# Kernel tuning notes

Hardware: AMD Instinct MI355X
Metric: run time of the kernel (lower is better)

## Reference

```python
import jax, jax.numpy as jnp
import numpy as np

B, K, N, D = 2, 384, 4096, 1024      # batch, filtered spans, all spans, dim_span
H, L, DD, NB = 150, 12, 20, 10       # scorer hidden, n_labels, dist emb dim, n buckets
REL_PROP, RESIDUAL, CTXT_FF = 2, True, True


def setup_inputs() -> dict:
    key = jax.random.key(0)
    ks = jax.random.split(key, 14)
    span_vecs = jax.random.normal(ks[0], (B, K, D), dtype=jnp.float32)
    all_span_vecs = jax.random.normal(ks[1], (B, N, D), dtype=jnp.float32)
    span_begin = jnp.sort(jax.random.randint(ks[2], (B, K), 0, 512), axis=-1)
    span_end = span_begin + jax.random.randint(ks[3], (B, K), 0, 8)
    span_lengths = jnp.full((B,), (K * 9) // 10, dtype=jnp.int32)
    valid = jnp.arange(K)[None, :] < span_lengths[:, None]
    square_mask = (valid[:, :, None] & valid[:, None, :]).astype(jnp.float32)
    prune_indices = jnp.sort(jax.random.randint(ks[4], (B, K), 0, N), axis=-1)
    sequence_lengths = jnp.full((B,), 512, dtype=jnp.int32)
    p = lambda k, sh: jax.random.normal(k, sh, dtype=jnp.float32) * 0.02
    return {
        'span_vecs': span_vecs, 'all_span_vecs': all_span_vecs,
        'span_begin': span_begin, 'span_end': span_end,
        'square_mask': square_mask, 'prune_indices': prune_indices,
        'span_lengths': span_lengths, 'sequence_lengths': sequence_lengths,
        'Wl': p(ks[5], (D, H)), 'bl': jnp.zeros((H,), jnp.float32),
        'Wr': p(ks[6], (D, H)), 'br': jnp.zeros((H,), jnp.float32),
        'dist_emb': p(ks[7], (NB, DD)),
        'Wd': p(ks[8], (DD, H)), 'bd': jnp.zeros((H,), jnp.float32),
        'Wo': p(ks[9], (H, L)), 'bo': jnp.zeros((L,), jnp.float32),
        'Wff1': p(ks[10], (3 * D, D)), 'Wff2': p(ks[11], (D, D)),
        'Wg': p(ks[12], (2 * D, D)), 'bg': jnp.zeros((D,), jnp.float32),
    }


def _bucket(d):
    # coref-style distance buckets: 0..4 exact, then log2 buckets up to NB-1
    da = jnp.abs(d)
    lg = jnp.floor(jnp.log2(jnp.maximum(da, 1).astype(jnp.float32))).astype(jnp.int32) + 3
    return jnp.where(da <= 4, da, jnp.minimum(lg, NB - 1)).astype(jnp.int32)


def _scorer(u, span_begin, span_end, Wl, bl, Wr, br, dist_emb, Wd, bd, Wo, bo):
    # OptFFpairs: pairwise FF scorer, [B,K,D] -> [B,K,K,L] (dropout = identity, eval mode)
    l = u @ Wl + bl                                          # [B,K,H]
    r = u @ Wr + br                                          # [B,K,H]
    dist = span_begin[:, None, :] - span_end[:, :, None]     # [B,K,K]
    d = dist_emb[_bucket(dist)] @ Wd + bd                    # [B,K,K,H]
    h = jax.nn.relu(l[:, :, None, :] + r[:, None, :, :] + d)
    return h @ Wo + bo                                       # [B,K,K,L]


def _forward(span_vecs, square_mask, span_begin, span_end,
             Wl, bl, Wr, br, dist_emb, Wd, bd, Wo, bo, Wff1, Wff2, Wg, bg):
    u = span_vecs
    scores = _scorer(u, span_begin, span_end, Wl, bl, Wr, br, dist_emb, Wd, bd, Wo, bo)
    for _ in range(REL_PROP):
        probs1 = jax.nn.sigmoid(scores.max(-1)) * square_mask       # [B,K,K]
        probs2 = jnp.swapaxes(probs1, 1, 2)
        ctxt1 = jnp.einsum('bij,bjd->bid', probs1, u) / (probs1.sum(-1) + 1e-7)[..., None]
        ctxt2 = jnp.einsum('bij,bjd->bid', probs2, u) / (probs2.sum(-1) + 1e-7)[..., None]
        if CTXT_FF:
            ctxt = jnp.tanh(jnp.concatenate((u, ctxt1, ctxt2), -1) @ Wff1) @ Wff2
        else:
            ctxt = ctxt1 + ctxt2
        g = jax.nn.sigmoid(jnp.concatenate((u, ctxt), -1) @ Wg + bg)  # MyGate
        u = g * u + (1.0 - g) * ctxt
        new_scores = _scorer(u, span_begin, span_end, Wl, bl, Wr, br, dist_emb, Wd, bd, Wo, bo)
        scores = scores + new_scores if RESIDUAL else new_scores
    return u, scores


def reference(span_vecs, all_span_vecs, span_begin, span_end, square_mask,
              prune_indices, span_lengths, sequence_lengths,
              Wl, bl, Wr, br, dist_emb, Wd, bd, Wo, bo, Wff1, Wff2, Wg, bg):
    u, scores = _forward(span_vecs, square_mask, span_begin, span_end,
                         Wl, bl, Wr, br, dist_emb, Wd, bd, Wo, bo, Wff1, Wff2, Wg, bg)
    # overwrite_spans: write updated filtered span vecs back into all-span tensor
    valid = jnp.arange(K)[None, :] < span_lengths[:, None]          # [B,K]
    bidx = jnp.broadcast_to(jnp.arange(B)[:, None], (B, K))
    cur = all_span_vecs[bidx, prune_indices]                        # [B,K,D]
    vals = jnp.where(valid[..., None], u, cur)                      # invalid -> no-op write
    update_all = all_span_vecs.at[bidx, prune_indices].set(vals)
    return update_all, u, scores
```

## Files before the change

kernel.cpp:

```cpp
#include <hip/hip_runtime.h>
#include <math.h>

constexpr int Bc = 2, Kc = 384, Nc = 4096, Dc = 1024;
constexpr int Hc = 150, Lc = 12, DDc = 20, NBc = 10;
constexpr int Mrows = Bc * Kc;

typedef __attribute__((ext_vector_type(8))) unsigned short ushort8;
typedef __attribute__((ext_vector_type(8))) short short8;
typedef __attribute__((ext_vector_type(4))) float f32x4;

__device__ __forceinline__ float sigmoidf_(float x) { return 1.0f / (1.0f + expf(-x)); }

__device__ __forceinline__ unsigned short f2b(float f) {
    unsigned u = __float_as_uint(f);
    unsigned r = (u + 0x7fffu + ((u >> 16) & 1u)) >> 16;
    return (unsigned short)r;
}
__device__ __forceinline__ float b2f(unsigned short u) {
    return __uint_as_float((unsigned)u << 16);
}

__global__ __launch_bounds__(256) void cvt_k(const float* __restrict__ s,
                                             unsigned short* __restrict__ d, int n) {
    for (int i = blockIdx.x * 256 + threadIdx.x; i < n; i += gridDim.x * 256)
        d[i] = f2b(s[i]);
}

__global__ __launch_bounds__(256) void dtab_k(const float* __restrict__ de,
                                              const float* __restrict__ Wd,
                                              const float* __restrict__ bd,
                                              float* __restrict__ dtab) {
    int idx = blockIdx.x * 256 + threadIdx.x;
    if (idx >= NBc * Hc) return;
    int n = idx / Hc, h = idx - n * Hc;
    float s = bd[h];
#pragma unroll
    for (int k = 0; k < DDc; ++k) s = fmaf(de[n * DDc + k], Wd[k * Hc + h], s);
    dtab[n * Hc + h] = s;
}

__global__ __launch_bounds__(256) void trw_k(const float* __restrict__ Wsrc,
                                             unsigned short* __restrict__ WT,
                                             int K, int N) {
    __shared__ unsigned short t[32][33];
    const int k0 = blockIdx.y * 32, n0 = blockIdx.x * 32;
    const int tx = threadIdx.x & 31, ty = threadIdx.x >> 5;
#pragma unroll
    for (int i = 0; i < 4; ++i)
        t[ty + i * 8][tx] = f2b(Wsrc[(size_t)(k0 + ty + i * 8) * N + n0 + tx]);
    __syncthreads();
#pragma unroll
    for (int i = 0; i < 4; ++i)
        WT[(size_t)(n0 + ty + i * 8) * K + k0 + tx] = t[tx][ty + i * 8];
}

__global__ __launch_bounds__(256) void trwlr_k(const float* __restrict__ Wl,
                                               const float* __restrict__ Wr,
                                               const float* __restrict__ bl,
                                               const float* __restrict__ br,
                                               unsigned short* __restrict__ WlrT,
                                               float* __restrict__ blr) {
    int idx = blockIdx.x * 256 + threadIdx.x;
    if (idx < Hc) { blr[idx] = bl[idx]; blr[Hc + idx] = br[idx]; }
    if (idx >= 2 * Hc * Dc) return;
    int r = idx >> 10, k = idx & 1023;
    float v = (r < Hc) ? Wl[(size_t)k * Hc + r] : Wr[(size_t)k * Hc + (r - Hc)];
    WlrT[idx] = f2b(v);
}

__global__ __launch_bounds__(256) void trb_k(const unsigned short* __restrict__ src,
                                             unsigned short* __restrict__ dst,
                                             int R, int C, long sBatch, long dBatch) {
    __shared__ unsigned short t[32][33];
    const int z = blockIdx.z;
    src += (size_t)z * sBatch;
    dst += (size_t)z * dBatch;
    const int r0 = blockIdx.y * 32, c0 = blockIdx.x * 32;
    const int tx = threadIdx.x & 31, ty = threadIdx.x >> 5;
#pragma unroll
    for (int i = 0; i < 4; ++i)
        t[ty + i * 8][tx] = src[(size_t)(r0 + ty + i * 8) * C + c0 + tx];
    __syncthreads();
#pragma unroll
    for (int i = 0; i < 4; ++i)
        dst[(size_t)(c0 + ty + i * 8) * R + r0 + tx] = t[tx][ty + i * 8];
}

template <int NSRC, int EPI, bool SPLITK, bool BTRANS>
__global__ __launch_bounds__(256) void mfma3(
    const unsigned short* __restrict__ a0, const unsigned short* __restrict__ a1,
    const unsigned short* __restrict__ a2, int arstride, long aBatch,
    const unsigned short* __restrict__ Bm, int bstride, long wBatch, int wmask,
    int N, int Kd, int chunk,
    const float* __restrict__ rs, long rsBatch,
    float* __restrict__ outf, unsigned short* __restrict__ outb, long oBatch) {
    constexpr int LDA = 72;
    __shared__ unsigned short Als[2][64 * LDA];
    __shared__ unsigned short Bls[2][64 * LDA];

    const int z = blockIdx.z;
    int kbeg;
    if (SPLITK) {
        kbeg = z * chunk;
        outf += (size_t)z * oBatch;
    } else {
        kbeg = 0;
        chunk = Kd;
        a0 += (size_t)z * aBatch;
        Bm += (size_t)(z & wmask) * wBatch;
        if (rs) rs += (size_t)z * rsBatch;
        if (outb) outb += (size_t)z * oBatch;
    }
    const int kend = kbeg + chunk;

    const int tid = threadIdx.x;
    const int wave = tid >> 6, lane = tid & 63;
    const int wr = wave >> 1, wc = wave & 1;
    const int l15 = lane & 15, lg = lane >> 4;
    const int row0 = blockIdx.y * 64, col0 = blockIdx.x * 64;
    const int srow = tid >> 2, skc = (tid & 3) * 16;

    f32x4 acc[2][2] = {};
    ushort8 ra0, ra1, rb0, rb1;

#define LOAD_SLAB(kb)                                                                  \
    {                                                                                  \
        int kglob = (kb) + skc;                                                        \
        const unsigned short* asrc = a0;                                               \
        int kl = kglob;                                                                \
        if (NSRC > 1) {                                                                \
            int s = kglob >> 10;                                                       \
            kl = kglob & 1023;                                                         \
            asrc = (s == 0) ? a0 : ((s == 1 || NSRC == 2) ? a1 : a2);                  \
        }                                                                              \
        const unsigned short* p = asrc + (size_t)(row0 + srow) * arstride + kl;        \
        ra0 = *(const ushort8*)p;                                                      \
        ra1 = *(const ushort8*)(p + 8);                                                \
        if (BTRANS) {                                                                  \
            const unsigned short* q = Bm + (size_t)((kb) + srow) * bstride + col0 + skc; \
            rb0 = *(const ushort8*)q;                                                  \
            rb1 = *(const ushort8*)(q + 8);                                            \
        } else {                                                                       \
            int col = col0 + srow;                                                     \
            if (col < N) {                                                             \
                const unsigned short* q = Bm + (size_t)col * bstride + kglob;          \
                rb0 = *(const ushort8*)q;                                              \
                rb1 = *(const ushort8*)(q + 8);                                        \
            } else {                                                                   \
                ushort8 z8 = {};                                                       \
                rb0 = z8;                                                              \
                rb1 = z8;                                                              \
            }                                                                          \
        }                                                                              \
    }

#define WRITE_SLAB(b)                                                                  \
    {                                                                                  \
        *(ushort8*)&Als[b][srow * LDA + skc] = ra0;                                    \
        *(ushort8*)&Als[b][srow * LDA + skc + 8] = ra1;                                \
        if (BTRANS) {                                                                  \
            _Pragma("unroll") for (int j = 0; j < 8; ++j)                              \
                Bls[b][(skc + j) * LDA + srow] = rb0[j];                               \
            _Pragma("unroll") for (int j = 0; j < 8; ++j)                              \
                Bls[b][(skc + 8 + j) * LDA + srow] = rb1[j];                           \
        } else {                                                                       \
            *(ushort8*)&Bls[b][srow * LDA + skc] = rb0;                                \
            *(ushort8*)&Bls[b][srow * LDA + skc + 8] = rb1;                            \
        }                                                                              \
    }

    LOAD_SLAB(kbeg);
    WRITE_SLAB(0);
    __syncthreads();

    int cur = 0;
    for (int k0 = kbeg; k0 < kend; k0 += 64) {
        const bool more = (k0 + 64 < kend);
        if (more) LOAD_SLAB(k0 + 64);
#pragma unroll
        for (int h = 0; h < 2; ++h) {
            short8 af0 = *(const short8*)&Als[cur][(wr * 32 + l15) * LDA + h * 32 + lg * 8];
            short8 af1 = *(const short8*)&Als[cur][(wr * 32 + 16 + l15) * LDA + h * 32 + lg * 8];
            short8 bf0 = *(const short8*)&Bls[cur][(wc * 32 + l15) * LDA + h * 32 + lg * 8];
            short8 bf1 = *(const short8*)&Bls[cur][(wc * 32 + 16 + l15) * LDA + h * 32 + lg * 8];
            acc[0][0] = __builtin_amdgcn_mfma_f32_16x16x32_bf16(af0, bf0, acc[0][0], 0, 0, 0);
            acc[0][1] = __builtin_amdgcn_mfma_f32_16x16x32_bf16(af0, bf1, acc[0][1], 0, 0, 0);
            acc[1][0] = __builtin_amdgcn_mfma_f32_16x16x32_bf16(af1, bf0, acc[1][0], 0, 0, 0);
            acc[1][1] = __builtin_amdgcn_mfma_f32_16x16x32_bf16(af1, bf1, acc[1][1], 0, 0, 0);
        }
        if (more) {
            int nb = cur ^ 1;
            WRITE_SLAB(nb);
            __syncthreads();
            cur = nb;
        }
    }
#undef LOAD_SLAB
#undef WRITE_SLAB

#pragma unroll
    for (int m = 0; m < 2; ++m)
#pragma unroll
        for (int n = 0; n < 2; ++n)
#pragma unroll
            for (int r = 0; r < 4; ++r) {
                int row = row0 + wr * 32 + m * 16 + lg * 4 + r;
                int col = col0 + wc * 32 + n * 16 + l15;
                if (col >= N) continue;
                size_t ix = (size_t)row * N + col;
                if (EPI == 5) outf[ix] = acc[m][n][r];
                else if (EPI == 4) outb[ix] = f2b(acc[m][n][r] * rs[row]);
            }
}

template <int ACT>
__global__ __launch_bounds__(256) void ep2_k(const float* __restrict__ PF, long pstride,
                                             const float* __restrict__ bias,
                                             const unsigned short* e1,
                                             const unsigned short* e2,
                                             float* outf, unsigned short* outb,
                                             int total, int N) {
    int idx = blockIdx.x * 256 + threadIdx.x;
    if (idx >= total) return;
    float v = PF[idx] + PF[pstride + idx] + PF[2 * pstride + idx] + PF[3 * pstride + idx];
    int col = idx - (idx / N) * N;
    if (ACT == 1) {
        outb[idx] = f2b(tanhf(v));
    } else if (ACT == 2) {
        outb[idx] = f2b(v);
    } else if (ACT == 3) {
        float g = sigmoidf_(v + bias[col]);
        float r = g * b2f(e1[idx]) + (1.0f - g) * b2f(e2[idx]);
        if (outf) outf[idx] = r;
        outb[idx] = f2b(r);
    } else if (ACT == 6) {
        outb[idx] = f2b(v + bias[col]);
    }
}

template <bool ADD>
__global__ __launch_bounds__(256) void scorer_k(const unsigned short* __restrict__ Lm,
                                                const unsigned short* __restrict__ Rm,
                                                int lst,
                                                const float* __restrict__ dtab,
                                                const int* __restrict__ sb,
                                                const int* __restrict__ se,
                                                const float* __restrict__ Wo,
                                                const float* __restrict__ bo,
                                                float* __restrict__ scores) {
    const int b = blockIdx.z;
    const int i0 = blockIdx.y * 16;
    const int j0 = blockIdx.x * 16;
    __shared__ float Ll[16 * 151];
    __shared__ float Rl[16 * 151];
    __shared__ float Dl[NBc * 151];
    __shared__ float Wol[Hc * Lc];
    __shared__ float bol[Lc];
    const int tid = threadIdx.x;
    for (int idx = tid; idx < 16 * Hc; idx += 256) {
        int r = idx / Hc, c = idx - r * Hc;
        Ll[r * 151 + c] = b2f(Lm[(size_t)(b * Kc + i0 + r) * lst + c]);
        Rl[r * 151 + c] = b2f(Rm[(size_t)(b * Kc + j0 + r) * lst + c]);
    }
    for (int idx = tid; idx < NBc * Hc; idx += 256) {
        int r = idx / Hc, c = idx - r * Hc;
        Dl[r * 151 + c] = dtab[r * Hc + c];
    }
    for (int idx = tid; idx < Hc * Lc; idx += 256) Wol[idx] = Wo[idx];
    if (tid < Lc) bol[tid] = bo[tid];
    __syncthreads();

    const int ty = tid >> 4, tx = tid & 15;
    const int i = i0 + ty, j = j0 + tx;
    int d = sb[b * Kc + j] - se[b * Kc + i];
    int da = d < 0 ? -d : d;
    int bucket = (da <= 4) ? da : min(31 - __clz(da) + 3, NBc - 1);
    const float* lp = &Ll[ty * 151];
    const float* rp = &Rl[tx * 151];
    const float* dp = &Dl[bucket * 151];
    float acc[Lc] = {};
    for (int h = 0; h < Hc; ++h) {
        float v = lp[h] + rp[h] + dp[h];
        v = fmaxf(v, 0.0f);
#pragma unroll
        for (int l = 0; l < Lc; ++l) acc[l] = fmaf(v, Wol[h * Lc + l], acc[l]);
    }
    size_t base = (((size_t)(b * Kc + i)) * Kc + j) * Lc;
#pragma unroll
    for (int l = 0; l < Lc; ++l) {
        float v = acc[l] + bol[l];
        if (ADD) v += scores[base + l];
        scores[base + l] = v;
    }
}

__global__ __launch_bounds__(256) void probs_k(const float* __restrict__ scores,
                                               const float* __restrict__ mask,
                                               unsigned short* __restrict__ PRbf) {
    int idx = blockIdx.x * 256 + threadIdx.x;
    if (idx >= Bc * Kc * Kc) return;
    const float* s = scores + (size_t)idx * Lc;
    float m = s[0];
#pragma unroll
    for (int l = 1; l < Lc; ++l) m = fmaxf(m, s[l]);
    PRbf[idx] = f2b(sigmoidf_(m) * mask[idx]);
}

__global__ __launch_bounds__(256) void rowsum_k(const unsigned short* __restrict__ probs,
                                                float* __restrict__ s1inv) {
    int row = (blockIdx.x * 256 + threadIdx.x) >> 6;
    int lane = threadIdx.x & 63;
    if (row >= Mrows) return;
    const unsigned short* p = probs + (size_t)row * Kc;
    float s = 0.0f;
    for (int j = lane; j < Kc; j += 64) s += b2f(p[j]);
#pragma unroll
    for (int off = 32; off > 0; off >>= 1) s += __shfl_down(s, off);
    if (lane == 0) s1inv[row] = 1.0f / (s + 1e-7f);
}

__global__ __launch_bounds__(256) void colsum_k(const unsigned short* __restrict__ probs,
                                                float* __restrict__ s2inv) {
    int idx = blockIdx.x * 256 + threadIdx.x;
    if (idx >= Mrows) return;
    int b = idx / Kc, j = idx - b * Kc;
    const unsigned short* p = probs + (size_t)b * Kc * Kc + j;
    float s = 0.0f;
    for (int i = 0; i < Kc; ++i) s += b2f(p[(size_t)i * Kc]);
    s2inv[idx] = 1.0f / (s + 1e-7f);
}

__global__ __launch_bounds__(256) void copy4_k(const float4* __restrict__ s,
                                               float4* __restrict__ d, int n4) {
    int i = blockIdx.x * 256 + threadIdx.x;
    if (i < n4) d[i] = s[i];
}

__global__ __launch_bounds__(256) void scatter_k(const float* __restrict__ Uf,
                                                 const int* __restrict__ pidx,
                                                 const int* __restrict__ slen,
                                                 float* __restrict__ out_all) {
    int bk = blockIdx.x;
    int b = bk / Kc, k = bk - b * Kc;
    if (k >= slen[b]) return;
    int idx = pidx[bk];
    if (k + 1 < Kc && pidx[bk + 1] == idx) return;
    const float4* s = (const float4*)(Uf + (size_t)bk * Dc);
    float4* d = (float4*)(out_all + ((size_t)b * Nc + idx) * Dc);
    for (int c = threadIdx.x; c < Dc / 4; c += 256) d[c] = s[c];
}

extern "C" void kernel_launch(void* const* d_in, const int* in_sizes, int n_in,
                              void* d_out, int out_size, void* d_ws, size_t ws_size,
                              hipStream_t stream) {
    const float* span_vecs = (const float*)d_in[0];
    const float* all_span_vecs = (const float*)d_in[1];
    const int* span_begin = (const int*)d_in[2];
    const int* span_end = (const int*)d_in[3];
    const float* square_mask = (const float*)d_in[4];
    const int* prune_indices = (const int*)d_in[5];
    const int* span_lengths = (const int*)d_in[6];
    const float* Wl = (const float*)d_in[8];
    const float* bl = (const float*)d_in[9];
    const float* Wr = (const float*)d_in[10];
    const float* br = (const float*)d_in[11];
    const float* dist_emb = (const float*)d_in[12];
    const float* Wd = (const float*)d_in[13];
    const float* bd = (const float*)d_in[14];
    const float* Wo = (const float*)d_in[15];
    const float* bo = (const float*)d_in[16];
    const float* Wff1 = (const float*)d_in[17];
    const float* Wff2 = (const float*)d_in[18];
    const float* Wg = (const float*)d_in[19];
    const float* bg = (const float*)d_in[20];

    float* out_all = (float*)d_out;
    float* out_u = out_all + (size_t)Bc * Nc * Dc;
    float* out_sc = out_u + (size_t)Mrows * Dc;

    float* w = out_all;
    float* DT = w;
    float* S1 = w + 1600;
    unsigned short* LRMb = (unsigned short*)(w + 3136);
    unsigned short* Ubf = (unsigned short*)(w + 118336);
    unsigned short* Cbf = (unsigned short*)(w + 511552);
    unsigned short* T1bf = (unsigned short*)(w + 1297984);
    unsigned short* PRbf = (unsigned short*)(w + 1494592);
    float* PF = w + 1789504;
    unsigned short* Wff1T = (unsigned short*)(w + 4935232);
    unsigned short* Wff2T = (unsigned short*)(w + 6508096);
    unsigned short* WgT = (unsigned short*)(w + 7032384);
    unsigned short* WlrT = (unsigned short*)(w + 8080960);
    float* blr = w + 8234560;
    const long KK = (long)Kc * Kc;
    const long KD = (long)Kc * Dc;
    unsigned short* C1bf = Cbf;
    unsigned short* C2bf = Cbf + 2 * KD;
    unsigned short* PT = PRbf + 2 * KK;
    unsigned short* CTbf = C1bf;
    const long PFS = (long)Mrows * Dc;

    dim3 blk(256);
    dim3 g_sc(Kc / 16, Kc / 16, Bc);
    dim3 g_ff(16, 12, 4);
    dim3 g_lr(5, 12, 4);
    dim3 g_pu(16, 6, 4);
    dim3 g_trp(12, 12, 2);

    cvt_k<<<2048, blk, 0, stream>>>(span_vecs, Ubf, Mrows * Dc);
    trw_k<<<dim3(32, 96), blk, 0, stream>>>(Wff1, Wff1T, 3 * Dc, Dc);
    trw_k<<<dim3(32, 32), blk, 0, stream>>>(Wff2, Wff2T, Dc, Dc);
    trw_k<<<dim3(32, 64), blk, 0, stream>>>(Wg, WgT, 2 * Dc, Dc);
    trwlr_k<<<(2 * Hc * Dc + 255) / 256, blk, 0, stream>>>(Wl, Wr, bl, br, WlrT, blr);
    dtab_k<<<(NBc * Hc + 255) / 256, blk, 0, stream>>>(dist_emb, Wd, bd, DT);

    const int TFF = Mrows * Dc;
    const int TLR = Mrows * 2 * Hc;

    mfma3<1, 5, true, false><<<g_lr, blk, 0, stream>>>(
        Ubf, nullptr, nullptr, Dc, 0, WlrT, Dc, 0, 0, 2 * Hc, Dc, 256,
        nullptr, 0, PF, nullptr, TLR);
    ep2_k<6><<<(TLR + 255) / 256, blk, 0, stream>>>(PF, TLR, blr, nullptr, nullptr,
                                                    nullptr, LRMb, TLR, 2 * Hc);
    scorer_k<false><<<g_sc, blk, 0, stream>>>(LRMb, LRMb + Hc, 2 * Hc, DT,
                                              span_begin, span_end, Wo, bo, out_sc);

    for (int it = 0; it < 2; ++it) {
        probs_k<<<(Bc * Kc * Kc + 255) / 256, blk, 0, stream>>>(out_sc, square_mask, PRbf);
        rowsum_k<<<Mrows / 4, blk, 0, stream>>>(PRbf, S1);
        colsum_k<<<(Mrows + 255) / 256, blk, 0, stream>>>(PRbf, S1 + Mrows);
        trb_k<<<g_trp, blk, 0, stream>>>(PRbf, PT, Kc, Kc, KK, KK);
        mfma3<1, 4, false, true><<<g_pu, blk, 0, stream>>>(
            PRbf, nullptr, nullptr, Kc, KK, Ubf, Dc, KD, 1, Dc, Kc, Kc,
            S1, Kc, nullptr, Cbf, KD);
        mfma3<3, 5, true, false><<<g_ff, blk, 0, stream>>>(
            Ubf, C1bf, C2bf, Dc, 0, Wff1T, 3 * Dc, 0, 0, Dc, 3 * Dc, 768,
            nullptr, 0, PF, nullptr, PFS);
        ep2_k<1><<<(TFF + 255) / 256, blk, 0, stream>>>(PF, PFS, nullptr, nullptr, nullptr,
                                                        nullptr, T1bf, TFF, Dc);
        mfma3<1, 5, true, false><<<g_ff, blk, 0, stream>>>(
            T1bf, nullptr, nullptr, Dc, 0, Wff2T, Dc, 0, 0, Dc, Dc, 256,
            nullptr, 0, PF, nullptr, PFS);
        ep2_k<2><<<(TFF + 255) / 256, blk, 0, stream>>>(PF, PFS, nullptr, nullptr, nullptr,
                                                        nullptr, CTbf, TFF, Dc);
        mfma3<2, 5, true, false><<<g_ff, blk, 0, stream>>>(
            Ubf, CTbf, nullptr, Dc, 0, WgT, 2 * Dc, 0, 0, Dc, 2 * Dc, 512,
            nullptr, 0, PF, nullptr, PFS);
        ep2_k<3><<<(TFF + 255) / 256, blk, 0, stream>>>(PF, PFS, bg, Ubf, CTbf,
                                                        (it == 1) ? out_u : nullptr,
                                                        Ubf, TFF, Dc);
        mfma3<1, 5, true, false><<<g_lr, blk, 0, stream>>>(
            Ubf, nullptr, nullptr, Dc, 0, WlrT, Dc, 0, 0, 2 * Hc, Dc, 256,
            nullptr, 0, PF, nullptr, TLR);
        ep2_k<6><<<(TLR + 255) / 256, blk, 0, stream>>>(PF, TLR, blr, nullptr, nullptr,
                                                        nullptr, LRMb, TLR, 2 * Hc);
        scorer_k<true><<<g_sc, blk, 0, stream>>>(LRMb, LRMb + Hc, 2 * Hc, DT,
                                                 span_begin, span_end, Wo, bo, out_sc);
    }

    copy4_k<<<((Bc * Nc * Dc / 4) + 255) / 256, blk, 0, stream>>>(
        (const float4*)all_span_vecs, (float4*)out_all, Bc * Nc * Dc / 4);
    scatter_k<<<Mrows, blk, 0, stream>>>(out_u, prune_indices, span_lengths, out_all);
}
```

Measured before the change: 456.0 us.

## Move pairwise scorer contraction onto bf16 MFMA instructions

```diff
diff --git a/kernel.cpp b/kernel.cpp
--- a/kernel.cpp
+++ b/kernel.cpp
@@ -239,58 +239,89 @@
 }
 
 template <bool ADD>
-__global__ __launch_bounds__(256) void scorer_k(const unsigned short* __restrict__ Lm,
-                                                const unsigned short* __restrict__ Rm,
-                                                int lst,
-                                                const float* __restrict__ dtab,
-                                                const int* __restrict__ sb,
-                                                const int* __restrict__ se,
-                                                const float* __restrict__ Wo,
-                                                const float* __restrict__ bo,
-                                                float* __restrict__ scores) {
+__global__ __launch_bounds__(256) void scorer2_k(
+    const unsigned short* __restrict__ Lm, const unsigned short* __restrict__ Rm,
+    int lst, const float* __restrict__ dtab,
+    const int* __restrict__ sb, const int* __restrict__ se,
+    const float* __restrict__ Wo, const float* __restrict__ bo,
+    float* __restrict__ scores) {
     const int b = blockIdx.z;
-    const int i0 = blockIdx.y * 16;
-    const int j0 = blockIdx.x * 16;
-    __shared__ float Ll[16 * 151];
-    __shared__ float Rl[16 * 151];
-    __shared__ float Dl[NBc * 151];
-    __shared__ float Wol[Hc * Lc];
-    __shared__ float bol[Lc];
+    const int i0 = blockIdx.y * 16, j0 = blockIdx.x * 16;
+    __shared__ unsigned short Lb[16 * 168];
+    __shared__ unsigned short Rb[16 * 168];
+    __shared__ float Df[10 * 164];
+    __shared__ int sbs[16];
     const int tid = threadIdx.x;
-    for (int idx = tid; idx < 16 * Hc; idx += 256) {
-        int r = idx / Hc, c = idx - r * Hc;
-        Ll[r * 151 + c] = b2f(Lm[(size_t)(b * Kc + i0 + r) * lst + c]);
-        Rl[r * 151 + c] = b2f(Rm[(size_t)(b * Kc + j0 + r) * lst + c]);
-    }
-    for (int idx = tid; idx < NBc * Hc; idx += 256) {
-        int r = idx / Hc, c = idx - r * Hc;
-        Dl[r * 151 + c] = dtab[r * Hc + c];
-    }
-    for (int idx = tid; idx < Hc * Lc; idx += 256) Wol[idx] = Wo[idx];
-    if (tid < Lc) bol[tid] = bo[tid];
+    const int wave = tid >> 6, lane = tid & 63;
+    const int l15 = lane & 15, lg = lane >> 4;
+
+    for (int idx = tid; idx < 16 * 160; idx += 256) {
+        int r = idx / 160, c = idx - r * 160;
+        Lb[r * 168 + c] = (c < Hc) ? Lm[(size_t)(b * Kc + i0 + r) * lst + c] : (unsigned short)0;
+        Rb[r * 168 + c] = (c < Hc) ? Rm[(size_t)(b * Kc + j0 + r) * lst + c] : (unsigned short)0;
+    }
+    for (int idx = tid; idx < 10 * 160; idx += 256) {
+        int r = idx / 160, c = idx - r * 160;
+        Df[r * 164 + c] = (c < Hc) ? dtab[r * Hc + c] : 0.0f;
+    }
+    if (tid < 16) sbs[tid] = sb[b * Kc + j0 + tid];
+
+    short8 bfr[5];
+#pragma unroll
+    for (int kc = 0; kc < 5; ++kc) {
+#pragma unroll
+        for (int j = 0; j < 8; ++j) {
+            int k = kc * 32 + lg * 8 + j;
+            float v = (k < Hc && l15 < Lc) ? Wo[k * Lc + l15] : 0.0f;
+            bfr[kc][j] = f2b(v);
+        }
+    }
+    const int se_i = se[b * Kc + i0 + l15];
+    const float bo_l = (l15 < Lc) ? bo[l15] : 0.0f;
     __syncthreads();
 
-    const int ty = tid >> 4, tx = tid & 15;
-    const int i = i0 + ty, j = j0 + tx;
-    int d = sb[b * Kc + j] - se[b * Kc + i];
-    int da = d < 0 ? -d : d;
-    int bucket = (da <= 4) ? da : min(31 - __clz(da) + 3, NBc - 1);
-    const float* lp = &Ll[ty * 151];
-    const float* rp = &Rl[tx * 151];
-    const float* dp = &Dl[bucket * 151];
-    float acc[Lc] = {};
-    for (int h = 0; h < Hc; ++h) {
-        float v = lp[h] + rp[h] + dp[h];
-        v = fmaxf(v, 0.0f);
-#pragma unroll
-        for (int l = 0; l < Lc; ++l) acc[l] = fmaf(v, Wol[h * Lc + l], acc[l]);
-    }
-    size_t base = (((size_t)(b * Kc + i)) * Kc + j) * Lc;
-#pragma unroll
-    for (int l = 0; l < Lc; ++l) {
-        float v = acc[l] + bol[l];
-        if (ADD) v += scores[base + l];
-        scores[base + l] = v;
+#pragma unroll
+    for (int t = 0; t < 4; ++t) {
+        const int jg = wave * 4 + t;
+        int d = sbs[jg] - se_i;
+        int da = d < 0 ? -d : d;
+        int bucket = (da <= 4) ? da : min(31 - __clz(da) + 3, NBc - 1);
+        const float* dp = &Df[bucket * 164];
+        f32x4 acc = {};
+#pragma unroll
+        for (int kc = 0; kc < 5; ++kc) {
+            int h0 = kc * 32 + lg * 8;
+            ushort8 La = *(const ushort8*)&Lb[l15 * 168 + h0];
+            ushort8 Ra = *(const ushort8*)&Rb[jg * 168 + h0];
+            f32x4 D0 = *(const f32x4*)&dp[h0];
+            f32x4 D1 = *(const f32x4*)&dp[h0 + 4];
+            const unsigned* lu = (const unsigned*)&La;
+            const unsigned* ru = (const unsigned*)&Ra;
+            union { unsigned u[4]; short8 s; } aw;
+#pragma unroll
+            for (int q = 0; q < 4; ++q) {
+                float de0 = (q < 2) ? D0[2 * q] : D1[2 * q - 4];
+                float de1 = (q < 2) ? D0[2 * q + 1] : D1[2 * q - 3];
+                float lv0 = __uint_as_float(lu[q] << 16);
+                float lv1 = __uint_as_float(lu[q] & 0xffff0000u);
+                float rv0 = __uint_as_float(ru[q] << 16);
+                float rv1 = __uint_as_float(ru[q] & 0xffff0000u);
+                float s0 = fmaxf(lv0 + rv0 + de0, 0.0f);
+                float s1 = fmaxf(lv1 + rv1 + de1, 0.0f);
+                aw.u[q] = (__float_as_uint(s0) >> 16) | (__float_as_uint(s1) & 0xffff0000u);
+            }
+            acc = __builtin_amdgcn_mfma_f32_16x16x32_bf16(aw.s, bfr[kc], acc, 0, 0, 0);
+        }
+        if (l15 < Lc) {
+#pragma unroll
+            for (int r = 0; r < 4; ++r) {
+                int irow = lg * 4 + r;
+                size_t off = (((size_t)(b * Kc + i0 + irow)) * Kc + (j0 + jg)) * Lc + l15;
+                float v = acc[r] + bo_l;
+                if (ADD) v += scores[off];
+                scores[off] = v;
+            }
+        }
     }
 }
 
@@ -422,8 +453,8 @@
         nullptr, 0, PF, nullptr, TLR);
     ep2_k<6><<<(TLR + 255) / 256, blk, 0, stream>>>(PF, TLR, blr, nullptr, nullptr,
                                                     nullptr, LRMb, TLR, 2 * Hc);
-    scorer_k<false><<<g_sc, blk, 0, stream>>>(LRMb, LRMb + Hc, 2 * Hc, DT,
-                                              span_begin, span_end, Wo, bo, out_sc);
+    scorer2_k<false><<<g_sc, blk, 0, stream>>>(LRMb, LRMb + Hc, 2 * Hc, DT,
+                                               span_begin, span_end, Wo, bo, out_sc);
 
     for (int it = 0; it < 2; ++it) {
         probs_k<<<(Bc * Kc * Kc + 255) / 256, blk, 0, stream>>>(out_sc, square_mask, PRbf);
@@ -454,8 +485,8 @@
             nullptr, 0, PF, nullptr, TLR);
         ep2_k<6><<<(TLR + 255) / 256, blk, 0, stream>>>(PF, TLR, blr, nullptr, nullptr,
                                                         nullptr, LRMb, TLR, 2 * Hc);
-        scorer_k<true><<<g_sc, blk, 0, stream>>>(LRMb, LRMb + Hc, 2 * Hc, DT,
-                                                 span_begin, span_end, Wo, bo, out_sc);
+        scorer2_k<true><<<g_sc, blk, 0, stream>>>(LRMb, LRMb + Hc, 2 * Hc, DT,
+                                                  span_begin, span_end, Wo, bo, out_sc);
     }
 
     copy4_k<<<((Bc * Nc * Dc / 4) + 255) / 256, blk, 0, stream>>>(
```

After: 424.0 us. -7.0%, faster.
